# Optimization experiments

Measured on AMD Instinct MI355X. Metric: run time of the kernel, lower is better.

The kernel has to match this reference:

```python
import jax, jax.numpy as jnp
import numpy as np
from jax import lax

TOL = 1e-06
POSINF = 1000000.0
NEGINF = -1000000.0


def _grad1(x, axis):
    """torch.gradient with spacing=1, edge_order=1 along `axis`:
    central differences in the interior, one-sided at the edges."""
    n = x.shape[axis]
    left = lax.slice_in_dim(x, 0, n - 2, axis=axis)
    right = lax.slice_in_dim(x, 2, n, axis=axis)
    interior = (right - left) * 0.5
    first = lax.slice_in_dim(x, 1, 2, axis=axis) - lax.slice_in_dim(x, 0, 1, axis=axis)
    last = lax.slice_in_dim(x, n - 1, n, axis=axis) - lax.slice_in_dim(x, n - 2, n - 1, axis=axis)
    return jnp.concatenate([first, interior, last], axis=axis)


def _clean(g):
    g = jnp.nan_to_num(g, nan=0.0, posinf=POSINF, neginf=NEGINF)
    return jnp.where(jnp.abs(g) < TOL, jnp.zeros_like(g), g)


def setup_inputs() -> dict:
    key = jax.random.key(0)
    k1, k2 = jax.random.split(key)
    shape = (8, 4, 64, 128, 128)  # [B, C=4, D, H, W]
    return {
        "input": jax.random.normal(k1, shape, dtype=jnp.float32),
        "target": jax.random.normal(k2, shape, dtype=jnp.float32),
    }


def reference(input, target):
    # spacing is ones per batch, so per-batch/per-channel loops collapse into
    # one vectorized finite-difference per spatial axis (dims 2, 3, 4).
    x = input.astype(jnp.float32)
    t = target.astype(jnp.float32)
    total = jnp.float32(0.0)
    for axis in (2, 3, 4):
        diff = _clean(_grad1(x, axis)) - _clean(_grad1(t, axis))
        # per-channel MSE (mean over b,d,h,w), then summed over the 4 channels
        total = total + jnp.sum(jnp.mean(diff * diff, axis=(0, 2, 3, 4)))
    return total
```

## Files before the change

kernel.cpp:

```cpp
#include <hip/hip_runtime.h>
#include <math.h>


#define Bn 8
#define Cn 4
#define Dn 64
#define Hn 128
#define Wn 128

static constexpr int NTOT = Bn * Cn * Dn * Hn * Wn;
static constexpr int NV4 = NTOT / 4;
static constexpr int NBLOCKS = 4096;
static constexpr int NTHREADS = 256;

__device__ __forceinline__ float cleanf(float g) {
    g = isnan(g) ? 0.0f : g;
    g = fminf(fmaxf(g, -1.0e6f), 1.0e6f);
    g = (fabsf(g) < 1.0e-6f) ? 0.0f : g;
    return g;
}

__device__ __forceinline__ float sqd(float gx, float gt) {
    float d = cleanf(gx) - cleanf(gt);
    return d * d;
}

__global__ __launch_bounds__(NTHREADS) void gradloss_main(
        const float* __restrict__ x, const float* __restrict__ t,
        double* __restrict__ partials) {
    const float4* __restrict__ X4 = (const float4*)x;
    const float4* __restrict__ T4 = (const float4*)t;

    float acc = 0.0f;
    const int stride = gridDim.x * blockDim.x;
    for (int i4 = blockIdx.x * blockDim.x + threadIdx.x; i4 < NV4; i4 += stride) {
        const int w4 = i4 & 31;
        const int h  = (i4 >> 5) & (Hn - 1);
        const int d  = (i4 >> 12) & (Dn - 1);

        const int hp = i4 + ((h < Hn - 1) ? 32 : 0);
        const int hm = i4 - ((h > 0) ? 32 : 0);
        const int dp = i4 + ((d < Dn - 1) ? 4096 : 0);
        const int dm = i4 - ((d > 0) ? 4096 : 0);
        const float sh = (h == 0 || h == Hn - 1) ? 1.0f : 0.5f;
        const float sd = (d == 0 || d == Dn - 1) ? 1.0f : 0.5f;

        const int li = 4 * i4 - ((w4 > 0) ? 1 : 0);
        const int ri = 4 * i4 + 3 + ((w4 < 31) ? 1 : 0);
        const float sw0 = (w4 == 0) ? 1.0f : 0.5f;
        const float sw3 = (w4 == 31) ? 1.0f : 0.5f;

        const float4 cx  = X4[i4],  ct  = T4[i4];
        const float4 xhp = X4[hp],  xhm = X4[hm];
        const float4 thp = T4[hp],  thm = T4[hm];
        const float4 xdp = X4[dp],  xdm = X4[dm];
        const float4 tdp = T4[dp],  tdm = T4[dm];
        const float  xl = x[li], xr = x[ri];
        const float  tl = t[li], tr = t[ri];

        acc += sqd((xhp.x - xhm.x) * sh, (thp.x - thm.x) * sh);
        acc += sqd((xhp.y - xhm.y) * sh, (thp.y - thm.y) * sh);
        acc += sqd((xhp.z - xhm.z) * sh, (thp.z - thm.z) * sh);
        acc += sqd((xhp.w - xhm.w) * sh, (thp.w - thm.w) * sh);

        acc += sqd((xdp.x - xdm.x) * sd, (tdp.x - tdm.x) * sd);
        acc += sqd((xdp.y - xdm.y) * sd, (tdp.y - tdm.y) * sd);
        acc += sqd((xdp.z - xdm.z) * sd, (tdp.z - tdm.z) * sd);
        acc += sqd((xdp.w - xdm.w) * sd, (tdp.w - tdm.w) * sd);

        acc += sqd((cx.y - xl) * sw0,   (ct.y - tl) * sw0);
        acc += sqd((cx.z - cx.x) * 0.5f, (ct.z - ct.x) * 0.5f);
        acc += sqd((cx.w - cx.y) * 0.5f, (ct.w - ct.y) * 0.5f);
        acc += sqd((xr - cx.z) * sw3,   (tr - ct.z) * sw3);
    }

    for (int off = 32; off > 0; off >>= 1)
        acc += __shfl_down(acc, off, 64);

    __shared__ float wsum[NTHREADS / 64];
    const int lane = threadIdx.x & 63;
    const int wid = threadIdx.x >> 6;
    if (lane == 0) wsum[wid] = acc;
    __syncthreads();
    if (threadIdx.x == 0) {
        double b = (double)wsum[0] + (double)wsum[1] +
                   (double)wsum[2] + (double)wsum[3];
        partials[blockIdx.x] = b;
    }
}

__global__ __launch_bounds__(256) void gradloss_reduce(
        const double* __restrict__ partials, float* __restrict__ out, int n) {
    double a = 0.0;
    for (int i = threadIdx.x; i < n; i += 256) a += partials[i];
    for (int off = 32; off > 0; off >>= 1)
        a += __shfl_down(a, off, 64);
    __shared__ double s[4];
    const int lane = threadIdx.x & 63;
    const int wid = threadIdx.x >> 6;
    if (lane == 0) s[wid] = a;
    __syncthreads();
    if (threadIdx.x == 0) {
        double tot = s[0] + s[1] + s[2] + s[3];
        out[0] = (float)(tot / 8388608.0);
    }
}

extern "C" void kernel_launch(void* const* d_in, const int* in_sizes, int n_in,
                              void* d_out, int out_size, void* d_ws, size_t ws_size,
                              hipStream_t stream) {
    const float* x = (const float*)d_in[0];
    const float* t = (const float*)d_in[1];
    float* out = (float*)d_out;
    double* partials = (double*)d_ws;

    gradloss_main<<<NBLOCKS, NTHREADS, 0, stream>>>(x, t, partials);
    gradloss_reduce<<<1, 256, 0, stream>>>(partials, out, NBLOCKS);
}
```

Baseline: 311.7 us.

## March threads along H with register rolling window and lane shuffles for W neighbors

```diff
diff --git a/kernel.cpp b/kernel.cpp
--- a/kernel.cpp
+++ b/kernel.cpp
@@ -8,10 +8,11 @@
 #define Hn 128
 #define Wn 128
 
-static constexpr int NTOT = Bn * Cn * Dn * Hn * Wn;
-static constexpr int NV4 = NTOT / 4;
-static constexpr int NBLOCKS = 4096;
+static constexpr int HCHUNK = 16;
 static constexpr int NTHREADS = 256;
+static constexpr int NBLOCKS = (32 * 64 * 8 * 32) / NTHREADS;
+static constexpr int ROW = Wn / 4;
+static constexpr int PLANE = Hn * ROW;
 
 __device__ __forceinline__ float cleanf(float g) {
     g = isnan(g) ? 0.0f : g;
@@ -26,52 +27,70 @@
 }
 
 __global__ __launch_bounds__(NTHREADS) void gradloss_main(
-        const float* __restrict__ x, const float* __restrict__ t,
+        const float* __restrict__ xf, const float* __restrict__ tf,
         double* __restrict__ partials) {
-    const float4* __restrict__ X4 = (const float4*)x;
-    const float4* __restrict__ T4 = (const float4*)t;
+    const int g = blockIdx.x * NTHREADS + threadIdx.x;
+    const int w4   = g & 31;
+    const int dlow = (g >> 5) & 7;
+    const int hc   = (g >> 8) & 7;
+    const int dhbc = g >> 11;
+    const int d    = ((dhbc & 7) << 3) + dlow;
+    const int bc   = dhbc >> 3;
+
+    const int h0 = hc * HCHUNK;
+    const int base = ((bc * Dn + d) * Hn + h0) * ROW + w4;
+    const float4* __restrict__ X = (const float4*)xf;
+    const float4* __restrict__ T = (const float4*)tf;
+    const float4* Xr = X + base;
+    const float4* Tr = T + base;
+
+    const int dpo = (d < Dn - 1) ? PLANE : 0;
+    const int dmo = (d > 0) ? -PLANE : 0;
+    const float sd  = (d == 0 || d == Dn - 1) ? 1.0f : 0.5f;
+    const float sw0 = (w4 == 0) ? 1.0f : 0.5f;
+    const float sw3 = (w4 == 31) ? 1.0f : 0.5f;
+
+    float4 xc = Xr[0], tc = Tr[0];
+    float4 xm, tm;
+    if (h0 > 0) { xm = Xr[-ROW]; tm = Tr[-ROW]; }
+    else        { xm = xc;       tm = tc; }
 
     float acc = 0.0f;
-    const int stride = gridDim.x * blockDim.x;
-    for (int i4 = blockIdx.x * blockDim.x + threadIdx.x; i4 < NV4; i4 += stride) {
-        const int w4 = i4 & 31;
-        const int h  = (i4 >> 5) & (Hn - 1);
-        const int d  = (i4 >> 12) & (Dn - 1);
+    #pragma unroll 4
+    for (int hl = 0; hl < HCHUNK; ++hl) {
+        const int h = h0 + hl;
+        const int po = (h < Hn - 1) ? ROW : 0;
+        const float4 xp  = Xr[po],  tp  = Tr[po];
+        const float4 xdp = Xr[dpo], xdm = Xr[dmo];
+        const float4 tdp = Tr[dpo], tdm = Tr[dmo];
+        const float sh = (h == 0 || h == Hn - 1) ? 1.0f : 0.5f;
 
-        const int hp = i4 + ((h < Hn - 1) ? 32 : 0);
-        const int hm = i4 - ((h > 0) ? 32 : 0);
-        const int dp = i4 + ((d < Dn - 1) ? 4096 : 0);
-        const int dm = i4 - ((d > 0) ? 4096 : 0);
-        const float sh = (h == 0 || h == Hn - 1) ? 1.0f : 0.5f;
-        const float sd = (d == 0 || d == Dn - 1) ? 1.0f : 0.5f;
-
-        const int li = 4 * i4 - ((w4 > 0) ? 1 : 0);
-        const int ri = 4 * i4 + 3 + ((w4 < 31) ? 1 : 0);
-        const float sw0 = (w4 == 0) ? 1.0f : 0.5f;
-        const float sw3 = (w4 == 31) ? 1.0f : 0.5f;
-
-        const float4 cx  = X4[i4],  ct  = T4[i4];
-        const float4 xhp = X4[hp],  xhm = X4[hm];
-        const float4 thp = T4[hp],  thm = T4[hm];
-        const float4 xdp = X4[dp],  xdm = X4[dm];
-        const float4 tdp = T4[dp],  tdm = T4[dm];
-        const float  xl = x[li], xr = x[ri];
-        const float  tl = t[li], tr = t[ri];
-
-        acc += sqd((xhp.x - xhm.x) * sh, (thp.x - thm.x) * sh);
-        acc += sqd((xhp.y - xhm.y) * sh, (thp.y - thm.y) * sh);
-        acc += sqd((xhp.z - xhm.z) * sh, (thp.z - thm.z) * sh);
-        acc += sqd((xhp.w - xhm.w) * sh, (thp.w - thm.w) * sh);
+        acc += sqd((xp.x - xm.x) * sh, (tp.x - tm.x) * sh);
+        acc += sqd((xp.y - xm.y) * sh, (tp.y - tm.y) * sh);
+        acc += sqd((xp.z - xm.z) * sh, (tp.z - tm.z) * sh);
+        acc += sqd((xp.w - xm.w) * sh, (tp.w - tm.w) * sh);
 
         acc += sqd((xdp.x - xdm.x) * sd, (tdp.x - tdm.x) * sd);
         acc += sqd((xdp.y - xdm.y) * sd, (tdp.y - tdm.y) * sd);
         acc += sqd((xdp.z - xdm.z) * sd, (tdp.z - tdm.z) * sd);
         acc += sqd((xdp.w - xdm.w) * sd, (tdp.w - tdm.w) * sd);
 
-        acc += sqd((cx.y - xl) * sw0,   (ct.y - tl) * sw0);
-        acc += sqd((cx.z - cx.x) * 0.5f, (ct.z - ct.x) * 0.5f);
-        acc += sqd((cx.w - cx.y) * 0.5f, (ct.w - ct.y) * 0.5f);
-        acc += sqd((xr - cx.z) * sw3,   (tr - ct.z) * sw3);
+        const float xlw = __shfl_up(xc.w, 1, 32);
+        const float tlw = __shfl_up(tc.w, 1, 32);
+        const float xrx = __shfl_down(xc.x, 1, 32);
+        const float trx = __shfl_down(tc.x, 1, 32);
+        const float xl = (w4 == 0)  ? xc.x : xlw;
+        const float tl = (w4 == 0)  ? tc.x : tlw;
+        const float xr = (w4 == 31) ? xc.w : xrx;
+        const float tr = (w4 == 31) ? tc.w : trx;
+
+        acc += sqd((xc.y - xl) * sw0,    (tc.y - tl) * sw0);
+        acc += sqd((xc.z - xc.x) * 0.5f, (tc.z - tc.x) * 0.5f);
+        acc += sqd((xc.w - xc.y) * 0.5f, (tc.w - tc.y) * 0.5f);
+        acc += sqd((xr - xc.z) * sw3,    (tr - tc.z) * sw3);
+
+        xm = xc; xc = xp; tm = tc; tc = tp;
+        Xr += ROW; Tr += ROW;
     }
 
     for (int off = 32; off > 0; off >>= 1)
```

Measured after the change: 288.7 us. 1.08x faster.
